# Optimization experiments

Measured on AMD Instinct MI355X. Metric: run time of the kernel, lower is better.

The kernel has to match this reference:

```python
import jax, jax.numpy as jnp
import numpy as np

B, S, D, H = 16, 1024, 768, 12
DH = D // H
DFF = 3072
EPS = 1e-5


def _layernorm(x, g, b):
    mu = jnp.mean(x, axis=-1, keepdims=True)
    var = jnp.mean(jnp.square(x - mu), axis=-1, keepdims=True)
    return (x - mu) * jax.lax.rsqrt(var + EPS) * g + b


def setup_inputs() -> dict:
    key = jax.random.key(0)
    ks = jax.random.split(key, 12)
    s = 0.02
    return {
        "x": jax.random.normal(ks[0], (B, S, D), jnp.float32),
        "ln1_g": jnp.ones((D,), jnp.float32),
        "ln1_b": jnp.zeros((D,), jnp.float32),
        "Wq": jax.random.normal(ks[1], (H, D, DH), jnp.float32) * s,
        "bq": jnp.zeros((H, DH), jnp.float32),
        "Wk": jax.random.normal(ks[2], (H, D, DH), jnp.float32) * s,
        "bk": jnp.zeros((H, DH), jnp.float32),
        "Wv": jax.random.normal(ks[3], (H, D, DH), jnp.float32) * s,
        "bv": jnp.zeros((H, DH), jnp.float32),
        "Wo": jax.random.normal(ks[4], (D, D), jnp.float32) * s,
        "bo": jnp.zeros((D,), jnp.float32),
        "ln2_g": jnp.ones((D,), jnp.float32),
        "ln2_b": jnp.zeros((D,), jnp.float32),
        "W1": jax.random.normal(ks[5], (D, DFF), jnp.float32) * s,
        "b1": jnp.zeros((DFF,), jnp.float32),
        "W2": jax.random.normal(ks[6], (DFF, D), jnp.float32) * s,
        "b2": jnp.zeros((D,), jnp.float32),
    }


def reference(x, ln1_g, ln1_b, Wq, bq, Wk, bk, Wv, bv, Wo, bo,
              ln2_g, ln2_b, W1, b1, W2, b2):
    # pre-norm MHA (all heads batched; equivalent to the per-head loop + concat)
    h = _layernorm(x, ln1_g, ln1_b)                           # [B,S,D]
    q = jnp.einsum('bsd,hdk->bhsk', h, Wq) + bq[None, :, None, :]
    k = jnp.einsum('bsd,hdk->bhsk', h, Wk) + bk[None, :, None, :]
    v = jnp.einsum('bsd,hdk->bhsk', h, Wv) + bv[None, :, None, :]
    scores = jnp.einsum('bhsk,bhtk->bhst', q, k) / jnp.sqrt(jnp.float32(DH))
    probs = jax.nn.softmax(scores, axis=-1)                   # [B,H,S,S]
    ctx = jnp.einsum('bhst,bhtk->bhsk', probs, v)             # [B,H,S,DH]
    ctx = ctx.transpose(0, 2, 1, 3).reshape(B, S, D)          # concat heads
    attn_out = ctx @ Wo + bo
    x = x + attn_out
    # pre-norm MLP (exact GELU, matching torch nn.GELU default)
    h2 = _layernorm(x, ln2_g, ln2_b)
    m = jax.nn.gelu(h2 @ W1 + b1, approximate=False) @ W2 + b2
    return x + m
```

## Files before the change

kernel.cpp:

```cpp
#include <hip/hip_runtime.h>
#include <hip/hip_bf16.h>
#include <math.h>

#define B_ 16
#define S_ 1024
#define D_ 768
#define H_ 12
#define DH_ 64
#define DFF 3072
#define M_ (B_*S_)

using short8 = __attribute__((ext_vector_type(8))) short;
using f32x4  = __attribute__((ext_vector_type(4))) float;

typedef __hip_bfloat16 bf16;

__device__ __forceinline__ bf16 f2b(float f) { return __float2bfloat16(f); }
__device__ __forceinline__ float ldf(const float* p) { return *p; }
__device__ __forceinline__ float ldf(const bf16* p) { return __bfloat162float(*p); }

__device__ __forceinline__ unsigned pkbf(float a, float b) {
  bf16 ha = f2b(a), hb = f2b(b);
  unsigned short ua = *(unsigned short*)&ha, ub = *(unsigned short*)&hb;
  return (unsigned)ua | ((unsigned)ub << 16);
}

__device__ __forceinline__ void gl2lds16(const void* g, void* l) {
  __builtin_amdgcn_global_load_lds((const __attribute__((address_space(1))) void*)g,
                                   (__attribute__((address_space(3))) void*)l, 16, 0, 0);
}

__global__ void conv_t(const float* __restrict__ in, bf16* __restrict__ out, int R, int C) {
  int tid = blockIdx.x * blockDim.x + threadIdx.x;
  if (tid >= R * C) return;
  int r = tid / C, c = tid - r * C;
  out[(size_t)c * R + r] = f2b(in[tid]);
}

__global__ void conv_wqkv(const float* __restrict__ Wq, const float* __restrict__ Wk,
                          const float* __restrict__ Wv, bf16* __restrict__ out) {
  int tid = blockIdx.x * blockDim.x + threadIdx.x;
  const int per = D_ * D_;
  if (tid >= 3 * per) return;
  const float* src = tid < per ? Wq : (tid < 2 * per ? Wk : Wv);
  int base = tid < per ? 0 : (tid < 2 * per ? D_ : 2 * D_);
  int rem = tid < per ? tid : (tid < 2 * per ? tid - per : tid - 2 * per);
  int h   = rem / (D_ * DH_);
  int rem2 = rem - h * (D_ * DH_);
  int d  = rem2 >> 6;
  int dh = rem2 & 63;
  out[(size_t)(base + h * DH_ + dh) * D_ + d] = f2b(src[rem]);
}

template <typename T>
__global__ __launch_bounds__(256) void ln_rows(const T* __restrict__ x,
                                               const float* __restrict__ g,
                                               const float* __restrict__ b,
                                               bf16* __restrict__ out, int rows) {
  int row  = blockIdx.x * 4 + (threadIdx.x >> 6);
  int lane = threadIdx.x & 63;
  if (row >= rows) return;
  const T* xr = x + (size_t)row * D_;
  float v[12];
  float sum = 0.f;
#pragma unroll
  for (int i = 0; i < 12; i++) { v[i] = ldf(xr + lane + i * 64); sum += v[i]; }
#pragma unroll
  for (int off = 32; off > 0; off >>= 1) sum += __shfl_xor(sum, off, 64);
  float mu = sum * (1.0f / 768.0f);
  float var = 0.f;
#pragma unroll
  for (int i = 0; i < 12; i++) { float d = v[i] - mu; var += d * d; }
#pragma unroll
  for (int off = 32; off > 0; off >>= 1) var += __shfl_xor(var, off, 64);
  var *= (1.0f / 768.0f);
  float rs = rsqrtf(var + 1e-5f);
  bf16* orow = out + (size_t)row * D_;
#pragma unroll
  for (int i = 0; i < 12; i++) {
    int c = lane + i * 64;
    orow[c] = f2b((v[i] - mu) * rs * g[c] + b[c]);
  }
}

#define GT 128
#define GK 32

template <int MODE>
__global__ __launch_bounds__(256) void gemm_bt(
    const bf16* __restrict__ A, const bf16* __restrict__ Bt, int K, int ldo,
    const float* __restrict__ bias0, const float* __restrict__ bias1,
    const float* __restrict__ bias2, const float* __restrict__ residf,
    const bf16* __restrict__ residb,
    float* __restrict__ outf, bf16* __restrict__ outb,
    bf16* __restrict__ qo, bf16* __restrict__ ko, bf16* __restrict__ vo) {
  __shared__ __align__(16) bf16 As[2][GT * GK];
  __shared__ __align__(16) bf16 Bs[2][GT * GK];
  const int tid  = threadIdx.x;
  const int w    = tid >> 6, lane = tid & 63;
  const int quad = lane >> 4, ln = lane & 15;
  const int lr   = lane >> 2, lc = (lane & 3) * 8;

  const int id = blockIdx.y * gridDim.x + blockIdx.x;
  const int bandY = gridDim.y >> 3;
  const int xcd = id & 7, loc = id >> 3;
  const int by = xcd * bandY + (loc % bandY);
  const int bx = loc / bandY;
  const int m0 = by * GT, n0 = bx * GT;
  const int wm = (w >> 1) * 64, wn = (w & 1) * 64;

  f32x4 acc[4][4];
#pragma unroll
  for (int i = 0; i < 4; i++)
#pragma unroll
    for (int j = 0; j < 4; j++)
#pragma unroll
      for (int r = 0; r < 4; r++) acc[i][j][r] = 0.f;

  const int T = K / GK;

  const bf16* gA0 = A  + (size_t)(m0 + w * 16 + lr) * K + lc;
  const bf16* gA1 = A  + (size_t)(m0 + 64 + w * 16 + lr) * K + lc;
  const bf16* gB0 = Bt + (size_t)(n0 + w * 16 + lr) * K + lc;
  const bf16* gB1 = Bt + (size_t)(n0 + 64 + w * 16 + lr) * K + lc;

  gl2lds16(gA0, &As[0][(w * 16) * GK]);
  gl2lds16(gA1, &As[0][(64 + w * 16) * GK]);
  gl2lds16(gB0, &Bs[0][(w * 16) * GK]);
  gl2lds16(gB1, &Bs[0][(64 + w * 16) * GK]);
  __syncthreads();

#pragma unroll 2
  for (int t = 0; t < T; t++) {
    if (t + 1 < T) {
      const int kk = (t + 1) * GK;
      bf16* An = As[(t + 1) & 1];
      bf16* Bn = Bs[(t + 1) & 1];
      gl2lds16(gA0 + kk, &An[(w * 16) * GK]);
      gl2lds16(gA1 + kk, &An[(64 + w * 16) * GK]);
      gl2lds16(gB0 + kk, &Bn[(w * 16) * GK]);
      gl2lds16(gB1 + kk, &Bn[(64 + w * 16) * GK]);
    }
    const bf16* Asc = As[t & 1];
    const bf16* Bsc = Bs[t & 1];
    short8 af[4], bfr[4];
#pragma unroll
    for (int u = 0; u < 4; u++) af[u]  = *(const short8*)&Asc[(wm + u * 16 + ln) * GK + quad * 8];
#pragma unroll
    for (int u = 0; u < 4; u++) bfr[u] = *(const short8*)&Bsc[(wn + u * 16 + ln) * GK + quad * 8];
#pragma unroll
    for (int i = 0; i < 4; i++)
#pragma unroll
      for (int j = 0; j < 4; j++)
        acc[i][j] = __builtin_amdgcn_mfma_f32_16x16x32_bf16(af[i], bfr[j], acc[i][j], 0, 0, 0);
    __syncthreads();
  }

#pragma unroll
  for (int i = 0; i < 4; i++) {
#pragma unroll
    for (int j = 0; j < 4; j++) {
#pragma unroll
      for (int r = 0; r < 4; r++) {
        const int m = m0 + wm + i * 16 + quad * 4 + r;
        const int n = n0 + wn + j * 16 + ln;
        float v = acc[i][j][r];
        if (MODE == 0) {
          const int b = m >> 10, s = m & 1023;
          if (n < D_) {
            int h = n >> 6, dh = n & 63;
            qo[(((size_t)(b * H_ + h)) * S_ + s) * DH_ + dh] = f2b(v + bias0[n]);
          } else if (n < 2 * D_) {
            int nn = n - D_; int h = nn >> 6, dh = nn & 63;
            ko[(((size_t)(b * H_ + h)) * S_ + s) * DH_ + dh] = f2b(v + bias1[nn]);
          } else {
            int nn = n - 2 * D_; int h = nn >> 6, dh = nn & 63;
            vo[(((size_t)(b * H_ + h)) * DH_ + dh) * S_ + s] = f2b(v + bias2[nn]);
          }
        } else if (MODE == 1) {
          outb[(size_t)m * ldo + n] = f2b(v + bias0[n] + residf[(size_t)m * ldo + n]);
        } else if (MODE == 2) {
          float z = v + bias0[n];
          float u = 0.7978845608028654f * z * (1.0f + 0.044715f * z * z);
          float e = __expf(2.0f * u);
          float th = 1.0f - 2.0f / (e + 1.0f);
          outb[(size_t)m * ldo + n] = f2b(0.5f * z * (1.0f + th));
        } else {
          outf[(size_t)m * ldo + n] =
              v + bias0[n] + __bfloat162float(residb[(size_t)m * ldo + n]);
        }
      }
    }
  }
}

#define KSTR 72
#define VSTR 136

__global__ __launch_bounds__(256) void attn(const bf16* __restrict__ qb,
                                            const bf16* __restrict__ kb,
                                            const bf16* __restrict__ vb,
                                            bf16* __restrict__ ctx) {
  __shared__ __align__(16) bf16 Kl[128 * KSTR];
  __shared__ __align__(16) bf16 Vl[64 * VSTR];
  const int blk = blockIdx.x;
  const int qt = blk & 7, bh = blk >> 3;
  const int b = bh / H_, h = bh - b * H_;
  const bf16* q  = qb + (size_t)bh * S_ * DH_;
  const bf16* kp = kb + (size_t)bh * S_ * DH_;
  const bf16* vp = vb + (size_t)bh * DH_ * S_;
  const int tid = threadIdx.x;
  const int w = tid >> 6, lane = tid & 63;
  const int quad = lane >> 4, ln = lane & 15;
  const int qs0 = qt * 128 + w * 32;

  const int krow = tid >> 3, kc = tid & 7;
  const int vrow = tid >> 4, vc = tid & 15;

  short8 kpre[4], vpre[4];
#pragma unroll
  for (int r = 0; r < 4; r++) {
    kpre[r] = *(const short8*)&kp[(size_t)(krow + r * 32) * DH_ + kc * 8];
    vpre[r] = *(const short8*)&vp[(size_t)(vrow + r * 16) * S_ + vc * 8];
  }

  short8 qf[2][2];
#pragma unroll
  for (int qg = 0; qg < 2; qg++)
#pragma unroll
    for (int ts = 0; ts < 2; ts++)
      qf[qg][ts] = *(const short8*)&q[(size_t)(qs0 + qg * 16 + ln) * DH_ + ts * 32 + quad * 8];

  f32x4 o[2][4];
  float mi[2], li[2];
#pragma unroll
  for (int qg = 0; qg < 2; qg++) {
    mi[qg] = -3.0e38f; li[qg] = 0.f;
#pragma unroll
    for (int dt = 0; dt < 4; dt++)
#pragma unroll
      for (int r = 0; r < 4; r++) o[qg][dt][r] = 0.f;
  }

  for (int t0 = 0; t0 < S_; t0 += 128) {
    __syncthreads();
#pragma unroll
    for (int r = 0; r < 4; r++) {
      *(short8*)&Kl[(krow + r * 32) * KSTR + kc * 8] = kpre[r];
      *(short8*)&Vl[(vrow + r * 16) * VSTR + vc * 8] = vpre[r];
    }
    const int tn = (t0 + 128) & (S_ - 1);
#pragma unroll
    for (int r = 0; r < 4; r++) {
      kpre[r] = *(const short8*)&kp[(size_t)(tn + krow + r * 32) * DH_ + kc * 8];
      vpre[r] = *(const short8*)&vp[(size_t)(vrow + r * 16) * S_ + tn + vc * 8];
    }
    __syncthreads();

    f32x4 sa[2][8];
#pragma unroll
    for (int qg = 0; qg < 2; qg++)
#pragma unroll
      for (int tt = 0; tt < 8; tt++)
#pragma unroll
        for (int r = 0; r < 4; r++) sa[qg][tt][r] = 0.f;
#pragma unroll
    for (int tt = 0; tt < 8; tt++) {
      short8 ka0 = *(const short8*)&Kl[(tt * 16 + ln) * KSTR + quad * 8];
      short8 ka1 = *(const short8*)&Kl[(tt * 16 + ln) * KSTR + 32 + quad * 8];
#pragma unroll
      for (int qg = 0; qg < 2; qg++) {
        sa[qg][tt] = __builtin_amdgcn_mfma_f32_16x16x32_bf16(ka0, qf[qg][0], sa[qg][tt], 0, 0, 0);
        sa[qg][tt] = __builtin_amdgcn_mfma_f32_16x16x32_bf16(ka1, qf[qg][1], sa[qg][tt], 0, 0, 0);
      }
    }

    unsigned pk[2][8][2];
#pragma unroll
    for (int qg = 0; qg < 2; qg++) {
      float mx = -3.0e38f;
#pragma unroll
      for (int tt = 0; tt < 8; tt++)
#pragma unroll
        for (int r = 0; r < 4; r++) {
          float s = sa[qg][tt][r] * 0.125f;
          sa[qg][tt][r] = s;
          mx = fmaxf(mx, s);
        }
      mx = fmaxf(mx, __shfl_xor(mx, 16, 64));
      mx = fmaxf(mx, __shfl_xor(mx, 32, 64));
      float mnew = fmaxf(mi[qg], mx);
      float alpha = __expf(mi[qg] - mnew);
      float rs = 0.f;
#pragma unroll
      for (int tt = 0; tt < 8; tt++) {
        float p0 = __expf(sa[qg][tt][0] - mnew);
        float p1 = __expf(sa[qg][tt][1] - mnew);
        float p2 = __expf(sa[qg][tt][2] - mnew);
        float p3 = __expf(sa[qg][tt][3] - mnew);
        rs += (p0 + p1) + (p2 + p3);
        pk[qg][tt][0] = pkbf(p0, p1);
        pk[qg][tt][1] = pkbf(p2, p3);
      }
      rs += __shfl_xor(rs, 16, 64);
      rs += __shfl_xor(rs, 32, 64);
      li[qg] = li[qg] * alpha + rs;
      mi[qg] = mnew;
#pragma unroll
      for (int dt = 0; dt < 4; dt++)
#pragma unroll
        for (int r = 0; r < 4; r++) o[qg][dt][r] *= alpha;
    }

    const int src = (quad & 1) * 32 + ln;
    const bool hi = quad >= 2;
#pragma unroll
    for (int tt32 = 0; tt32 < 4; tt32++) {
#pragma unroll
      for (int qg = 0; qg < 2; qg++) {
        unsigned e0 = pk[qg][2 * tt32][0],     e1 = pk[qg][2 * tt32][1];
        unsigned o0 = pk[qg][2 * tt32 + 1][0], o1 = pk[qg][2 * tt32 + 1][1];
        unsigned a0 = __shfl((int)e0, src, 64),      b0 = __shfl((int)o0, src, 64);
        unsigned a1 = __shfl((int)e1, src, 64),      b1 = __shfl((int)o1, src, 64);
        unsigned a2 = __shfl((int)e0, src + 16, 64), b2 = __shfl((int)o0, src + 16, 64);
        unsigned a3 = __shfl((int)e1, src + 16, 64), b3 = __shfl((int)o1, src + 16, 64);
        union { unsigned u[4]; short8 s; } fr;
        fr.u[0] = hi ? b0 : a0;
        fr.u[1] = hi ? b1 : a1;
        fr.u[2] = hi ? b2 : a2;
        fr.u[3] = hi ? b3 : a3;
#pragma unroll
        for (int dt = 0; dt < 4; dt++) {
          short8 va = *(const short8*)&Vl[(dt * 16 + ln) * VSTR + tt32 * 32 + quad * 8];
          o[qg][dt] = __builtin_amdgcn_mfma_f32_16x16x32_bf16(va, fr.s, o[qg][dt], 0, 0, 0);
        }
      }
    }
  }

  __syncthreads();
  bf16* Ol = Kl;
#pragma unroll
  for (int qg = 0; qg < 2; qg++) {
    float inv = 1.0f / li[qg];
#pragma unroll
    for (int dt = 0; dt < 4; dt++)
#pragma unroll
      for (int r = 0; r < 4; r++)
        Ol[(w * 32 + qg * 16 + ln) * KSTR + dt * 16 + quad * 4 + r] = f2b(o[qg][dt][r] * inv);
  }
  __syncthreads();
  const int orow = tid >> 3, oc = tid & 7;
#pragma unroll
  for (int rd = 0; rd < 4; rd++) {
    int row = orow + rd * 32;
    short8 val = *(const short8*)&Ol[row * KSTR + oc * 8];
    *(short8*)&ctx[((size_t)(b * S_ + qt * 128 + row)) * D_ + h * DH_ + oc * 8] = val;
  }
}

extern "C" void kernel_launch(void* const* d_in, const int* in_sizes, int n_in,
                              void* d_out, int out_size, void* d_ws, size_t ws_size,
                              hipStream_t stream) {
  const float* x    = (const float*)d_in[0];
  const float* ln1g = (const float*)d_in[1];
  const float* ln1b = (const float*)d_in[2];
  const float* Wq   = (const float*)d_in[3];
  const float* bq   = (const float*)d_in[4];
  const float* Wk   = (const float*)d_in[5];
  const float* bk   = (const float*)d_in[6];
  const float* Wv   = (const float*)d_in[7];
  const float* bv   = (const float*)d_in[8];
  const float* Wo   = (const float*)d_in[9];
  const float* bo   = (const float*)d_in[10];
  const float* ln2g = (const float*)d_in[11];
  const float* ln2b = (const float*)d_in[12];
  const float* W1   = (const float*)d_in[13];
  const float* b1   = (const float*)d_in[14];
  const float* W2   = (const float*)d_in[15];
  const float* b2   = (const float*)d_in[16];

  char* ws = (char*)d_ws;
  const size_t SZ_MD = (size_t)M_ * D_ * 2;
  size_t off = 0;
  bf16* wqkvt = (bf16*)(ws + off); off += (size_t)3 * D_ * D_ * 2;
  bf16* wot   = (bf16*)(ws + off); off += (size_t)D_ * D_ * 2;
  bf16* w1t   = (bf16*)(ws + off); off += (size_t)DFF * D_ * 2;
  bf16* w2t   = (bf16*)(ws + off); off += (size_t)D_ * DFF * 2;
  bf16* h     = (bf16*)(ws + off); off += SZ_MD;
  bf16* x1    = (bf16*)(ws + off); off += SZ_MD;
  char* unionbase = ws + off;
  bf16* qbuf = (bf16*)(unionbase);
  bf16* kbuf = (bf16*)(unionbase + SZ_MD);
  bf16* vbuf = (bf16*)(unionbase + 2 * SZ_MD);
  bf16* ctx  = (bf16*)(unionbase + 3 * SZ_MD);
  bf16* a1   = (bf16*)(unionbase);

  conv_wqkv<<<(3 * D_ * D_ + 255) / 256, 256, 0, stream>>>(Wq, Wk, Wv, wqkvt);
  conv_t<<<(D_ * D_ + 255) / 256, 256, 0, stream>>>(Wo, wot, D_, D_);
  conv_t<<<(D_ * DFF + 255) / 256, 256, 0, stream>>>(W1, w1t, D_, DFF);
  conv_t<<<(D_ * DFF + 255) / 256, 256, 0, stream>>>(W2, w2t, DFF, D_);
  ln_rows<float><<<M_ / 4, 256, 0, stream>>>(x, ln1g, ln1b, h, M_);

  gemm_bt<0><<<dim3(3 * D_ / GT, M_ / GT), 256, 0, stream>>>(
      h, wqkvt, D_, 0, bq, bk, bv, nullptr, nullptr, nullptr, nullptr,
      qbuf, kbuf, vbuf);

  attn<<<B_ * H_ * (S_ / 128), 256, 0, stream>>>(qbuf, kbuf, vbuf, ctx);

  gemm_bt<1><<<dim3(D_ / GT, M_ / GT), 256, 0, stream>>>(
      ctx, wot, D_, D_, bo, nullptr, nullptr, x, nullptr, nullptr, x1,
      nullptr, nullptr, nullptr);

  ln_rows<bf16><<<M_ / 4, 256, 0, stream>>>(x1, ln2g, ln2b, h, M_);
  gemm_bt<2><<<dim3(DFF / GT, M_ / GT), 256, 0, stream>>>(
      h, w1t, D_, DFF, b1, nullptr, nullptr, nullptr, nullptr, nullptr, a1,
      nullptr, nullptr, nullptr);

  gemm_bt<3><<<dim3(D_ / GT, M_ / GT), 256, 0, stream>>>(
      a1, w2t, DFF, D_, b2, nullptr, nullptr, nullptr, x1, (float*)d_out,
      nullptr, nullptr, nullptr, nullptr);
}
```

Before: 751.0 us.

## Use 512-thread GEMM blocks with register-prefetched global loads instead of LDS DMA

```diff
diff --git a/kernel.cpp b/kernel.cpp
--- a/kernel.cpp
+++ b/kernel.cpp
@@ -23,11 +23,6 @@
   bf16 ha = f2b(a), hb = f2b(b);
   unsigned short ua = *(unsigned short*)&ha, ub = *(unsigned short*)&hb;
   return (unsigned)ua | ((unsigned)ub << 16);
-}
-
-__device__ __forceinline__ void gl2lds16(const void* g, void* l) {
-  __builtin_amdgcn_global_load_lds((const __attribute__((address_space(1))) void*)g,
-                                   (__attribute__((address_space(3))) void*)l, 16, 0, 0);
 }
 
 __global__ void conv_t(const float* __restrict__ in, bf16* __restrict__ out, int R, int C) {
@@ -87,7 +82,7 @@
 #define GK 32
 
 template <int MODE>
-__global__ __launch_bounds__(256) void gemm_bt(
+__global__ __launch_bounds__(512, 4) void gemm_bt(
     const bf16* __restrict__ A, const bf16* __restrict__ Bt, int K, int ldo,
     const float* __restrict__ bias0, const float* __restrict__ bias1,
     const float* __restrict__ bias2, const float* __restrict__ residf,
@@ -99,7 +94,6 @@
   const int tid  = threadIdx.x;
   const int w    = tid >> 6, lane = tid & 63;
   const int quad = lane >> 4, ln = lane & 15;
-  const int lr   = lane >> 2, lc = (lane & 3) * 8;
 
   const int id = blockIdx.y * gridDim.x + blockIdx.x;
   const int bandY = gridDim.y >> 3;
@@ -107,59 +101,60 @@
   const int by = xcd * bandY + (loc % bandY);
   const int bx = loc / bandY;
   const int m0 = by * GT, n0 = bx * GT;
-  const int wm = (w >> 1) * 64, wn = (w & 1) * 64;
-
-  f32x4 acc[4][4];
+  const int wm = (w >> 2) * 64, wn = (w & 3) * 32;
+
+  const int ar = tid >> 2;
+  const int ac = (tid & 3) * 8;
+
+  f32x4 acc[4][2];
 #pragma unroll
   for (int i = 0; i < 4; i++)
 #pragma unroll
-    for (int j = 0; j < 4; j++)
+    for (int j = 0; j < 2; j++)
 #pragma unroll
       for (int r = 0; r < 4; r++) acc[i][j][r] = 0.f;
 
   const int T = K / GK;
 
-  const bf16* gA0 = A  + (size_t)(m0 + w * 16 + lr) * K + lc;
-  const bf16* gA1 = A  + (size_t)(m0 + 64 + w * 16 + lr) * K + lc;
-  const bf16* gB0 = Bt + (size_t)(n0 + w * 16 + lr) * K + lc;
-  const bf16* gB1 = Bt + (size_t)(n0 + 64 + w * 16 + lr) * K + lc;
-
-  gl2lds16(gA0, &As[0][(w * 16) * GK]);
-  gl2lds16(gA1, &As[0][(64 + w * 16) * GK]);
-  gl2lds16(gB0, &Bs[0][(w * 16) * GK]);
-  gl2lds16(gB1, &Bs[0][(64 + w * 16) * GK]);
+  short8 apre, bpre;
+  apre = *(const short8*)&A[(size_t)(m0 + ar) * K + ac];
+  bpre = *(const short8*)&Bt[(size_t)(n0 + ar) * K + ac];
+  *(short8*)&As[0][ar * GK + ac] = apre;
+  *(short8*)&Bs[0][ar * GK + ac] = bpre;
+  apre = *(const short8*)&A[(size_t)(m0 + ar) * K + GK + ac];
+  bpre = *(const short8*)&Bt[(size_t)(n0 + ar) * K + GK + ac];
   __syncthreads();
 
 #pragma unroll 2
   for (int t = 0; t < T; t++) {
-    if (t + 1 < T) {
-      const int kk = (t + 1) * GK;
-      bf16* An = As[(t + 1) & 1];
-      bf16* Bn = Bs[(t + 1) & 1];
-      gl2lds16(gA0 + kk, &An[(w * 16) * GK]);
-      gl2lds16(gA1 + kk, &An[(64 + w * 16) * GK]);
-      gl2lds16(gB0 + kk, &Bn[(w * 16) * GK]);
-      gl2lds16(gB1 + kk, &Bn[(64 + w * 16) * GK]);
-    }
     const bf16* Asc = As[t & 1];
     const bf16* Bsc = Bs[t & 1];
-    short8 af[4], bfr[4];
+    short8 af[4], bfr[2];
 #pragma unroll
     for (int u = 0; u < 4; u++) af[u]  = *(const short8*)&Asc[(wm + u * 16 + ln) * GK + quad * 8];
 #pragma unroll
-    for (int u = 0; u < 4; u++) bfr[u] = *(const short8*)&Bsc[(wn + u * 16 + ln) * GK + quad * 8];
+    for (int u = 0; u < 2; u++) bfr[u] = *(const short8*)&Bsc[(wn + u * 16 + ln) * GK + quad * 8];
 #pragma unroll
     for (int i = 0; i < 4; i++)
 #pragma unroll
-      for (int j = 0; j < 4; j++)
+      for (int j = 0; j < 2; j++)
         acc[i][j] = __builtin_amdgcn_mfma_f32_16x16x32_bf16(af[i], bfr[j], acc[i][j], 0, 0, 0);
-    __syncthreads();
+    if (t + 1 < T) {
+      bf16* Asn = As[(t + 1) & 1];
+      bf16* Bsn = Bs[(t + 1) & 1];
+      *(short8*)&Asn[ar * GK + ac] = apre;
+      *(short8*)&Bsn[ar * GK + ac] = bpre;
+      const int kn = (t + 2 < T) ? (t + 2) * GK : 0;
+      apre = *(const short8*)&A[(size_t)(m0 + ar) * K + kn + ac];
+      bpre = *(const short8*)&Bt[(size_t)(n0 + ar) * K + kn + ac];
+      __syncthreads();
+    }
   }
 
 #pragma unroll
   for (int i = 0; i < 4; i++) {
 #pragma unroll
-    for (int j = 0; j < 4; j++) {
+    for (int j = 0; j < 2; j++) {
 #pragma unroll
       for (int r = 0; r < 4; r++) {
         const int m = m0 + wm + i * 16 + quad * 4 + r;
@@ -402,22 +397,22 @@
   conv_t<<<(D_ * DFF + 255) / 256, 256, 0, stream>>>(W2, w2t, DFF, D_);
   ln_rows<float><<<M_ / 4, 256, 0, stream>>>(x, ln1g, ln1b, h, M_);
 
-  gemm_bt<0><<<dim3(3 * D_ / GT, M_ / GT), 256, 0, stream>>>(
+  gemm_bt<0><<<dim3(3 * D_ / GT, M_ / GT), 512, 0, stream>>>(
       h, wqkvt, D_, 0, bq, bk, bv, nullptr, nullptr, nullptr, nullptr,
       qbuf, kbuf, vbuf);
 
   attn<<<B_ * H_ * (S_ / 128), 256, 0, stream>>>(qbuf, kbuf, vbuf, ctx);
 
-  gemm_bt<1><<<dim3(D_ / GT, M_ / GT), 256, 0, stream>>>(
+  gemm_bt<1><<<dim3(D_ / GT, M_ / GT), 512, 0, stream>>>(
       ctx, wot, D_, D_, bo, nullptr, nullptr, x, nullptr, nullptr, x1,
       nullptr, nullptr, nullptr);
 
   ln_rows<bf16><<<M_ / 4, 256, 0, stream>>>(x1, ln2g, ln2b, h, M_);
-  gemm_bt<2><<<dim3(DFF / GT, M_ / GT), 256, 0, stream>>>(
+  gemm_bt<2><<<dim3(DFF / GT, M_ / GT), 512, 0, stream>>>(
       h, w1t, D_, DFF, b1, nullptr, nullptr, nullptr, nullptr, nullptr, a1,
       nullptr, nullptr, nullptr);
 
-  gemm_bt<3><<<dim3(D_ / GT, M_ / GT), 256, 0, stream>>>(
+  gemm_bt<3><<<dim3(D_ / GT, M_ / GT), 512, 0, stream>>>(
       a1, w2t, DFF, D_, b2, nullptr, nullptr, nullptr, x1, (float*)d_out,
       nullptr, nullptr, nullptr, nullptr);
 }
```

After: 663.7 us. -11.6%, faster.
